# Kernel optimization log

Measured on AMD Instinct MI355X. Metric: run time of the kernel, lower is better.

The kernel has to match this reference:

```python
import jax, jax.numpy as jnp
import numpy as np

EMBED_DIM = 128
NUM_HEADS = 16
HEAD_DIM = EMBED_DIM // NUM_HEADS
SCALE = HEAD_DIM ** -0.5


def setup_inputs() -> dict:
    key = jax.random.key(0)
    ks = jax.random.split(key, 9)
    B, S, E = 4, 2048, EMBED_DIM
    s = 1.0 / np.sqrt(E)
    return {
        "x": jax.random.normal(ks[0], (B, S, E), dtype=jnp.float32),
        "Wq": jax.random.uniform(ks[1], (E, E), jnp.float32, -s, s),
        "bq": jax.random.uniform(ks[2], (E,), jnp.float32, -s, s),
        "Wk": jax.random.uniform(ks[3], (E, E), jnp.float32, -s, s),
        "bk": jax.random.uniform(ks[4], (E,), jnp.float32, -s, s),
        "Wv": jax.random.uniform(ks[5], (E, E), jnp.float32, -s, s),
        "bv": jax.random.uniform(ks[6], (E,), jnp.float32, -s, s),
        "Wo": jax.random.uniform(ks[7], (E, E), jnp.float32, -s, s),
        "bo": jax.random.uniform(ks[8], (E,), jnp.float32, -s, s),
    }


def reference(x, Wq, bq, Wk, bk, Wv, bv, Wo, bo):
    B, S, E = x.shape
    H, D = NUM_HEADS, HEAD_DIM
    # projections (torch Linear: x @ W.T + b)
    q = (x @ Wq.T + bq).reshape(B, S, H, D).transpose(0, 2, 1, 3)  # [B,H,S,D]
    k = (x @ Wk.T + bk).reshape(B, S, H, D).transpose(0, 2, 1, 3)
    v = (x @ Wv.T + bv).reshape(B, S, H, D).transpose(0, 2, 1, 3)
    scores = jnp.einsum("bhqd,bhkd->bhqk", q, k) * SCALE  # [B,H,S,S]
    causal_mask = jnp.triu(jnp.ones((S, S), dtype=bool), k=1)  # True above diag
    scores = jnp.where(causal_mask, jnp.float32(-1e9), scores)
    w = jax.nn.sigmoid(scores)
    w = w / jnp.sum(w, axis=-1, keepdims=True)  # sigmoid-sum normalization
    attn = jnp.einsum("bhqk,bhkd->bhqd", w, v)  # [B,H,S,D]
    attn = attn.transpose(0, 2, 1, 3).reshape(B, S, E)
    return attn @ Wo.T + bo
```

## Files before the change

### kernel.cpp

```cpp
#include <hip/hip_runtime.h>
#include <math.h>

#define EDIM 128
#define NHEAD 16
#define HDIM 8
#define SEQ 2048
#define BATCH 4
#define NROW (BATCH*SEQ)
#define QNEG (-0.35355339059327373f * 1.4426950408889634f)

#if __has_builtin(__builtin_amdgcn_exp2f)
#define EXP2F(x) __builtin_amdgcn_exp2f(x)
#else
#define EXP2F(x) exp2f(x)
#endif
#define RCPF(x) __builtin_amdgcn_rcpf(x)

typedef __attribute__((ext_vector_type(8))) short short8v;
typedef __attribute__((ext_vector_type(4))) short short4v;
typedef __attribute__((ext_vector_type(4))) float float4v;

union U16x8 { uint4 u; short8v s; };
union U16x4 { uint2 u; short4v s; };

#if __has_builtin(__builtin_amdgcn_mfma_f32_16x16x16bf16_1k)
#define MFMA_PV(a,b,c) __builtin_amdgcn_mfma_f32_16x16x16bf16_1k(a,b,c,0,0,0)
#else
static __device__ __forceinline__ float4v mfma_pv_asm(short4v a, short4v b, float4v c) {
  float4v d;
  asm("v_mfma_f32_16x16x16_bf16 %0, %1, %2, %3" : "=v"(d) : "v"(a), "v"(b), "v"(c));
  return d;
}
#define MFMA_PV(a,b,c) mfma_pv_asm(a,b,c)
#endif

__device__ __forceinline__ unsigned pk_bf16(float a, float b) {
  unsigned ua = __float_as_uint(a), ub = __float_as_uint(b);
  unsigned lo = (ua + 0x7fffu + ((ua >> 16) & 1u)) >> 16;
  unsigned hi = (ub + 0x7fffu + ((ub >> 16) & 1u)) & 0xffff0000u;
  return lo | hi;
}

__device__ __forceinline__
void afrags(const unsigned short* xs, int lq, int qd, short8v a[4])
{
  #pragma unroll
  for (int kk = 0; kk < 4; ++kk) {
    const unsigned addr =
        (unsigned)(lq * 256 + kk * 64 + qd * 16) ^ (unsigned)((lq & 7) << 4);
    a[kk] = *(const short8v*)((const char*)xs + addr);
  }
}

template<int MODE>
__device__ __forceinline__
void proj32(const float* __restrict__ X, const float* __restrict__ W,
            const float* __restrict__ bias, void* __restrict__ out,
            int row0, int tid,
            unsigned short* wlds, unsigned short* xs, unsigned short* bnc)
{
  {
    const int n = tid >> 1, h = (tid & 1) * 64;
    const float4* src = (const float4*)(W + (size_t)n * EDIM + h);
    const unsigned xr = (unsigned)((n & 7) << 4);
    #pragma unroll
    for (int j = 0; j < 8; ++j) {
      const float4 f0 = src[2 * j], f1 = src[2 * j + 1];
      const uint4 v = make_uint4(pk_bf16(f0.x, f0.y), pk_bf16(f0.z, f0.w),
                                 pk_bf16(f1.x, f1.y), pk_bf16(f1.z, f1.w));
      *(uint4*)((char*)wlds + ((unsigned)(n * 256 + h * 2 + j * 16) ^ xr)) = v;
    }
  }
  {
    const int r = tid >> 3, c = tid & 7;
    const float4* src = (const float4*)(X + (size_t)(row0 + r) * EDIM + c * 16);
    const unsigned xr = (unsigned)((r & 7) << 4);
    const float4 f0 = src[0], f1 = src[1], f2 = src[2], f3 = src[3];
    const uint4 v0 = make_uint4(pk_bf16(f0.x, f0.y), pk_bf16(f0.z, f0.w),
                                pk_bf16(f1.x, f1.y), pk_bf16(f1.z, f1.w));
    const uint4 v1 = make_uint4(pk_bf16(f2.x, f2.y), pk_bf16(f2.z, f2.w),
                                pk_bf16(f3.x, f3.y), pk_bf16(f3.z, f3.w));
    *(uint4*)((char*)xs + ((unsigned)(r * 256 + c * 32) ^ xr)) = v0;
    *(uint4*)((char*)xs + ((unsigned)(r * 256 + c * 32 + 16) ^ xr)) = v1;
  }
  __syncthreads();

  const int lane = tid & 63, wv = tid >> 6;
  const int lq = lane & 15, qd = lane >> 4;
  const int n0 = wv * 32;

  short8v b0[4], b1[4];
  #pragma unroll
  for (int kk = 0; kk < 4; ++kk) {
    const unsigned ad = (unsigned)((n0 + lq) * 256 + kk * 64 + qd * 16)
                      ^ (unsigned)((lq & 7) << 4);
    b0[kk] = *(const short8v*)((const char*)wlds + ad);
    b1[kk] = *(const short8v*)((const char*)wlds + ad + 4096);
  }

  const int nA = n0 + lq, nB = nA + 16;
  const float bzA = bias[nA], bzB = bias[nB];
  const int b_ = row0 >> 11;

  #pragma unroll
  for (int rt = 0; rt < 2; ++rt) {
    const int rowt = row0 + rt * 16;
    short8v a[4];
    afrags(xs + rt * 2048, lq, qd, a);

    float4v D0 = {0.f, 0.f, 0.f, 0.f}, D1 = {0.f, 0.f, 0.f, 0.f};
    #pragma unroll
    for (int kk = 0; kk < 4; ++kk) {
      D0 = __builtin_amdgcn_mfma_f32_16x16x32_bf16(a[kk], b0[kk], D0, 0, 0, 0);
      D1 = __builtin_amdgcn_mfma_f32_16x16x32_bf16(a[kk], b1[kk], D1, 0, 0, 0);
    }

    if (MODE == 3) {
      float* of = (float*)out + (size_t)(rowt + qd * 4) * EDIM + nA;
      #pragma unroll
      for (int r = 0; r < 4; ++r) {
        of[r * EDIM]      = D0[r] + bzA;
        of[r * EDIM + 16] = D1[r] + bzB;
      }
      continue;
    }

    const int srel = rowt & (SEQ - 1);

    if (MODE == 2) {
      const int tg = srel >> 4;
      unsigned short* oU = (unsigned short*)out;
      {
        const int bh = b_ * NHEAD + (nA >> 3), dv = nA & 7;
        uint2 p;
        p.x = pk_bf16(D0[0] + bzA, D0[1] + bzA);
        p.y = pk_bf16(D0[2] + bzA, D0[3] + bzA);
        *(uint2*)(oU + (size_t)bh * (SEQ * HDIM) + tg * 128 + dv * 16 + qd * 4) = p;
      }
      {
        const int bh = b_ * NHEAD + (nB >> 3), dv = nB & 7;
        uint2 p;
        p.x = pk_bf16(D1[0] + bzB, D1[1] + bzB);
        p.y = pk_bf16(D1[2] + bzB, D1[3] + bzB);
        *(uint2*)(oU + (size_t)bh * (SEQ * HDIM) + tg * 128 + dv * 16 + qd * 4) = p;
      }
      continue;
    }

    #pragma unroll
    for (int r = 0; r < 4; ++r) {
      float vA = D0[r] + bzA, vB = D1[r] + bzB;
      if (MODE == 0) { vA *= QNEG; vB *= QNEG; }
      const int m = qd * 4 + r;
      bnc[m * 20 + lq]       = (unsigned short)pk_bf16(vA, 0.f);
      bnc[320 + m * 20 + lq] = (unsigned short)pk_bf16(vB, 0.f);
    }
    __syncthreads();

    const int mm   = lane & 15;
    const int half = (lane >> 4) & 1;
    const int tile = lane >> 5;
    const unsigned short* sp = bnc + tile * 320 + mm * 20 + half * 8;
    const uint2 w0 = *(const uint2*)sp;
    const uint2 w1 = *(const uint2*)(sp + 4);
    const int bh = b_ * NHEAD + wv * 4 + tile * 2 + half;
    unsigned short* dp = (unsigned short*)out + ((size_t)bh * SEQ + srel + mm) * 8;
    *(uint4*)dp = make_uint4(w0.x, w0.y, w1.x, w1.y);
    __syncthreads();
  }
}

__global__ __launch_bounds__(256)
void qkv_kernel(const float* __restrict__ X,
                const float* __restrict__ Wq, const float* __restrict__ Wk,
                const float* __restrict__ Wv,
                const float* __restrict__ bq, const float* __restrict__ bk,
                const float* __restrict__ bv,
                unsigned* __restrict__ qb, unsigned* __restrict__ kb,
                unsigned* __restrict__ vb)
{
  __shared__ __align__(16) unsigned short wlds[16384];
  __shared__ __align__(16) unsigned short xs[4096];
  __shared__ __align__(16) unsigned short bnc[4 * 640];
  const int tid = threadIdx.x;
  const int row0 = blockIdx.x * 32;
  unsigned short* myb = bnc + (tid >> 6) * 640;
  const int m = blockIdx.y;
  if (m == 0)      proj32<0>(X, Wq, bq, (void*)qb, row0, tid, wlds, xs, myb);
  else if (m == 1) proj32<1>(X, Wk, bk, (void*)kb, row0, tid, wlds, xs, myb);
  else             proj32<2>(X, Wv, bv, (void*)vb, row0, tid, wlds, xs, myb);
}

__global__ __launch_bounds__(256)
void oproj_kernel(const float* __restrict__ A, const float* __restrict__ Wo,
                  const float* __restrict__ bo, float* __restrict__ out)
{
  __shared__ __align__(16) unsigned short wlds[16384];
  __shared__ __align__(16) unsigned short xs[4096];
  proj32<3>(A, Wo, bo, (void*)out, blockIdx.x * 32, threadIdx.x, wlds, xs, nullptr);
}

template<bool DIAG>
__device__ __forceinline__
float4v attn_step(short8v kf, short8v qf, short4v vf, float4v acc,
                  int laneq, int quad)
{
  const float4v z = {0.f, 0.f, 0.f, 0.f};
  float4v st = __builtin_amdgcn_mfma_f32_16x16x32_bf16(kf, qf, z, 0, 0, 0);
  unsigned rb[4];
  #pragma unroll
  for (int r = 0; r < 4; ++r) {
    float s = RCPF(1.f + EXP2F(st[r]));
    if (DIAG) s = (4 * quad + r <= laneq) ? s : 0.f;
    rb[r] = __float_as_uint(s) + 0x8000u;
  }
  U16x4 p;
  p.u.x = __builtin_amdgcn_perm(rb[1], rb[0], 0x07060302u);
  p.u.y = __builtin_amdgcn_perm(rb[3], rb[2], 0x07060302u);
  return MFMA_PV(p.s, vf, acc);
}

__device__ __forceinline__
short4v load_vfrag(const unsigned short* __restrict__ Vtbh, int t,
                   int quad, int d, bool is8)
{
  const unsigned short* p = Vtbh + t * 128 + d * 16 + 4 * quad;
  const uint2 v = *(const uint2*)p;
  U16x4 vf;
  vf.u.x = is8 ? 0x3F803F80u : v.x;
  vf.u.y = is8 ? 0x3F803F80u : v.y;
  return vf.s;
}

__device__ __forceinline__
void epilogue(float4v acc, int T, int bh, int laneq, int quad,
              float* __restrict__ out)
{
  const int b_ = bh >> 4, h = bh & 15;
  const int pidx = (quad * 16 + 8) << 2;
  #pragma unroll
  for (int r = 0; r < 4; ++r) {
    const float den = __int_as_float(
        __builtin_amdgcn_ds_bpermute(pidx, __float_as_int(acc[r])));
    const float val = acc[r] * RCPF(den);
    const int row = 16 * T + 4 * quad + r;
    if (laneq < 8)
      out[(size_t)(b_ * SEQ + row) * EDIM + h * HDIM + laneq] = val;
  }
}

__global__ __launch_bounds__(128, 8)
void attn_kernel(const unsigned* __restrict__ Qb, const unsigned* __restrict__ Kb,
                 const unsigned* __restrict__ Vb, float* __restrict__ out)
{
  __shared__ float cmb[2][64][4];

  const int bh    = blockIdx.x & 63;
  const int g     = blockIdx.x >> 6;
  const int w     = threadIdx.x >> 6;
  const int lane  = threadIdx.x & 63;
  const int laneq = lane & 15;
  const int quad  = lane >> 4;
  const int L = g, H = 127 - g;
  const int mL = (L + 1) >> 1, mH = (H + 1) >> 1;
  const int d   = laneq & 7;
  const bool is8 = (laneq == 8);

  const uint4* Kg = (const uint4*)Kb + (size_t)bh * 2048;
  const uint4* Qg = (const uint4*)Qb + (size_t)bh * 2048;
  const unsigned short* Vtbh = (const unsigned short*)Vb + (size_t)bh * SEQ * HDIM;

  U16x8 qfl, qfh;
  {
    const uint4 rl = Qg[16 * L + laneq];
    const uint4 rh = Qg[16 * H + laneq];
    qfl.u = (lane < 16) ? rl : make_uint4(0u, 0u, 0u, 0u);
    qfh.u = (lane < 16) ? rh : make_uint4(0u, 0u, 0u, 0u);
  }

  float4v accL = {0.f, 0.f, 0.f, 0.f};
  float4v accH = {0.f, 0.f, 0.f, 0.f};

  if (w == 0) {
    U16x8 kf; kf.u = Kg[laneq];
    short4v vf = load_vfrag(Vtbh, 0, quad, d, is8);
    #pragma unroll 2
    for (int t = 0; t < mH; ++t) {
      U16x8 kn; kn.u = Kg[16 * (t + 1) + laneq];
      short4v vn = load_vfrag(Vtbh, t + 1, quad, d, is8);
      if (t < mL) accL = attn_step<false>(kf.s, qfl.s, vf, accL, laneq, quad);
      accH = attn_step<false>(kf.s, qfh.s, vf, accH, laneq, quad);
      kf = kn; vf = vn;
    }
  } else {
    U16x8 kf; kf.u = Kg[16 * mL + laneq];
    short4v vf = load_vfrag(Vtbh, mL, quad, d, is8);
    #pragma unroll 2
    for (int t = mL; t < L; ++t) {
      U16x8 kn; kn.u = Kg[16 * (t + 1) + laneq];
      short4v vn = load_vfrag(Vtbh, t + 1, quad, d, is8);
      accL = attn_step<false>(kf.s, qfl.s, vf, accL, laneq, quad);
      kf = kn; vf = vn;
    }
    accL = attn_step<true>(kf.s, qfl.s, vf, accL, laneq, quad);
    kf.u = Kg[16 * mH + laneq];
    vf = load_vfrag(Vtbh, mH, quad, d, is8);
    #pragma unroll 2
    for (int t = mH; t < H; ++t) {
      U16x8 kn; kn.u = Kg[16 * (t + 1) + laneq];
      short4v vn = load_vfrag(Vtbh, t + 1, quad, d, is8);
      accH = attn_step<false>(kf.s, qfh.s, vf, accH, laneq, quad);
      kf = kn; vf = vn;
    }
    accH = attn_step<true>(kf.s, qfh.s, vf, accH, laneq, quad);

    *(float4*)&cmb[0][lane][0] = make_float4(accL[0], accL[1], accL[2], accL[3]);
    *(float4*)&cmb[1][lane][0] = make_float4(accH[0], accH[1], accH[2], accH[3]);
  }
  __syncthreads();

  if (w == 0) {
    const float4 pL = *(const float4*)&cmb[0][lane][0];
    const float4 pH = *(const float4*)&cmb[1][lane][0];
    accL[0] += pL.x; accL[1] += pL.y; accL[2] += pL.z; accL[3] += pL.w;
    accH[0] += pH.x; accH[1] += pH.y; accH[2] += pH.z; accH[3] += pH.w;
    epilogue(accL, L, bh, laneq, quad, out);
    epilogue(accH, H, bh, laneq, quad, out);
  }
}

extern "C" void kernel_launch(void* const* d_in, const int* in_sizes, int n_in,
                              void* d_out, int out_size, void* d_ws, size_t ws_size,
                              hipStream_t stream)
{
  const float* x  = (const float*)d_in[0];
  const float* Wq = (const float*)d_in[1];
  const float* bq = (const float*)d_in[2];
  const float* Wk = (const float*)d_in[3];
  const float* bk = (const float*)d_in[4];
  const float* Wv = (const float*)d_in[5];
  const float* bv = (const float*)d_in[6];
  const float* Wo = (const float*)d_in[7];
  const float* bo = (const float*)d_in[8];

  float* ws = (float*)d_ws;
  float*    attn = ws + 65536;
  unsigned* Qb   = (unsigned*)(ws + 65536 + 1048576);
  unsigned* Kb   = Qb + (size_t)524288;
  unsigned* Vb   = Kb + (size_t)524288;

  qkv_kernel<<<dim3(NROW / 32, 3), 256, 0, stream>>>(x, Wq, Wk, Wv, bq, bk, bv,
                                                     Qb, Kb, Vb);
  attn_kernel<<<dim3(4096), 128, 0, stream>>>(Qb, Kb, Vb, attn);
  oproj_kernel<<<dim3(NROW / 32), 256, 0, stream>>>(attn, Wo, bo, (float*)d_out);
}
```

Measured before the change: 121.8 us.

## Switch attention to 32x32x16 MFMA tiles with permlane32 swap for P

Rewrites the attention kernel to use 32x32 query/key tiles with the 32x32x16 bf16 MFMA for both scores and P·V, using permlane32_swap to rearrange the sigmoid probabilities into A-operand layout. Each block now handles a pair of 32-row tiles, and the combined key range is split evenly across two waves. This halves the grid, and the larger tiles are meant to raise MFMA efficiency per load. In exchange the kernel carries 16-register accumulators, lowers the occupancy hint to 4, and drops the explicit software prefetch of K/V.

```diff
diff --git a/kernel.cpp b/kernel.cpp
--- a/kernel.cpp
+++ b/kernel.cpp
@@ -19,26 +19,35 @@
 typedef __attribute__((ext_vector_type(8))) short short8v;
 typedef __attribute__((ext_vector_type(4))) short short4v;
 typedef __attribute__((ext_vector_type(4))) float float4v;
+typedef __attribute__((ext_vector_type(16))) float float16v;
 
 union U16x8 { uint4 u; short8v s; };
 union U16x4 { uint2 u; short4v s; };
 
-#if __has_builtin(__builtin_amdgcn_mfma_f32_16x16x16bf16_1k)
-#define MFMA_PV(a,b,c) __builtin_amdgcn_mfma_f32_16x16x16bf16_1k(a,b,c,0,0,0)
+#define MFMA32(a,b,c) __builtin_amdgcn_mfma_f32_32x32x16_bf16(a,b,c,0,0,0)
+
+__device__ __forceinline__ void lane32swap(unsigned &x, unsigned &y) {
+#if __has_builtin(__builtin_amdgcn_permlane32_swap)
+  typedef __attribute__((ext_vector_type(2))) unsigned uint2v;
+  uint2v r = __builtin_amdgcn_permlane32_swap(x, y, false, false);
+  x = r[0]; y = r[1];
 #else
-static __device__ __forceinline__ float4v mfma_pv_asm(short4v a, short4v b, float4v c) {
-  float4v d;
-  asm("v_mfma_f32_16x16x16_bf16 %0, %1, %2, %3" : "=v"(d) : "v"(a), "v"(b), "v"(c));
-  return d;
-}
-#define MFMA_PV(a,b,c) mfma_pv_asm(a,b,c)
+  asm volatile("v_permlane32_swap_b32 %0, %1" : "+v"(x), "+v"(y));
 #endif
+}
 
 __device__ __forceinline__ unsigned pk_bf16(float a, float b) {
   unsigned ua = __float_as_uint(a), ub = __float_as_uint(b);
   unsigned lo = (ua + 0x7fffu + ((ua >> 16) & 1u)) >> 16;
   unsigned hi = (ub + 0x7fffu + ((ub >> 16) & 1u)) & 0xffff0000u;
   return lo | hi;
+}
+
+__device__ __forceinline__ float16v zero16() {
+  float16v z;
+  #pragma unroll
+  for (int i = 0; i < 16; ++i) z[i] = 0.f;
+  return z;
 }
 
 __device__ __forceinline__
@@ -202,130 +211,145 @@
 
 template<bool DIAG>
 __device__ __forceinline__
-float4v attn_step(short8v kf, short8v qf, short4v vf, float4v acc,
-                  int laneq, int quad)
-{
-  const float4v z = {0.f, 0.f, 0.f, 0.f};
-  float4v st = __builtin_amdgcn_mfma_f32_16x16x32_bf16(kf, qf, z, 0, 0, 0);
-  unsigned rb[4];
-  #pragma unroll
-  for (int r = 0; r < 4; ++r) {
-    float s = RCPF(1.f + EXP2F(st[r]));
-    if (DIAG) s = (4 * quad + r <= laneq) ? s : 0.f;
-    rb[r] = __float_as_uint(s) + 0x8000u;
-  }
-  U16x4 p;
-  p.u.x = __builtin_amdgcn_perm(rb[1], rb[0], 0x07060302u);
-  p.u.y = __builtin_amdgcn_perm(rb[3], rb[2], 0x07060302u);
-  return MFMA_PV(p.s, vf, acc);
-}
-
-__device__ __forceinline__
-short4v load_vfrag(const unsigned short* __restrict__ Vtbh, int t,
-                   int quad, int d, bool is8)
-{
-  const unsigned short* p = Vtbh + t * 128 + d * 16 + 4 * quad;
-  const uint2 v = *(const uint2*)p;
-  U16x4 vf;
-  vf.u.x = is8 ? 0x3F803F80u : v.x;
-  vf.u.y = is8 ? 0x3F803F80u : v.y;
-  return vf.s;
-}
-
-__device__ __forceinline__
-void epilogue(float4v acc, int T, int bh, int laneq, int quad,
-              float* __restrict__ out)
+float16v step32(const uint4* __restrict__ Kg,
+                const unsigned short* __restrict__ Vtbh,
+                int t, U16x8 qf, float16v acc,
+                int lane, unsigned voff, bool is8)
+{
+  U16x8 kf; kf.u = Kg[32 * t + (lane & 31)];
+  const unsigned short* vt = Vtbh + 256 * t;
+  U16x8 v1, v2;
+  {
+    const uint4 a = *(const uint4*)(vt + voff);
+    const uint4 b = *(const uint4*)(vt + 128 + voff);
+    const uint4 ones = make_uint4(0x3F803F80u, 0x3F803F80u,
+                                  0x3F803F80u, 0x3F803F80u);
+    v1.u = is8 ? ones : a;
+    v2.u = is8 ? ones : b;
+  }
+
+  float16v st = MFMA32(kf.s, qf.s, zero16());
+
+  unsigned u[8];
+  #pragma unroll
+  for (int i = 0; i < 8; ++i) {
+    float s0 = RCPF(1.f + EXP2F(st[2 * i]));
+    float s1 = RCPF(1.f + EXP2F(st[2 * i + 1]));
+    if (DIAG) {
+      const int rb = ((2 * i) & 3) + 8 * (i >> 1) + ((lane >> 5) << 2);
+      const int q_ = lane & 31;
+      s0 = (rb     <= q_) ? s0 : 0.f;
+      s1 = (rb + 1 <= q_) ? s1 : 0.f;
+    }
+    const unsigned b0 = __float_as_uint(s0) + 0x8000u;
+    const unsigned b1 = __float_as_uint(s1) + 0x8000u;
+    u[i] = __builtin_amdgcn_perm(b1, b0, 0x07060302u);
+  }
+
+  lane32swap(u[0], u[2]);
+  lane32swap(u[1], u[3]);
+  lane32swap(u[4], u[6]);
+  lane32swap(u[5], u[7]);
+
+  U16x8 pa, pb;
+  pa.u = make_uint4(u[0], u[1], u[2], u[3]);
+  pb.u = make_uint4(u[4], u[5], u[6], u[7]);
+  acc = MFMA32(pa.s, v1.s, acc);
+  acc = MFMA32(pb.s, v2.s, acc);
+  return acc;
+}
+
+__device__ __forceinline__
+void seg32(const uint4* __restrict__ Kg, const unsigned short* __restrict__ Vtbh,
+           U16x8 qf, int T, int a, int b, float16v &acc,
+           int lane, unsigned voff, bool is8)
+{
+  if (a >= b) return;
+  const bool hasDiag = (b == T + 1);
+  const int e = hasDiag ? b - 1 : b;
+  for (int t = a; t < e; ++t)
+    acc = step32<false>(Kg, Vtbh, t, qf, acc, lane, voff, is8);
+  if (hasDiag)
+    acc = step32<true>(Kg, Vtbh, T, qf, acc, lane, voff, is8);
+}
+
+__device__ __forceinline__
+void epilogue32(float16v acc, int T, int bh, int lane, float* __restrict__ out)
 {
   const int b_ = bh >> 4, h = bh & 15;
-  const int pidx = (quad * 16 + 8) << 2;
-  #pragma unroll
-  for (int r = 0; r < 4; ++r) {
+  const int n = lane & 31;
+  const int pidx = ((lane & 32) | 8) << 2;
+  const int rowb = 32 * T + ((lane >> 5) << 2);
+  #pragma unroll
+  for (int reg = 0; reg < 16; ++reg) {
     const float den = __int_as_float(
-        __builtin_amdgcn_ds_bpermute(pidx, __float_as_int(acc[r])));
-    const float val = acc[r] * RCPF(den);
-    const int row = 16 * T + 4 * quad + r;
-    if (laneq < 8)
-      out[(size_t)(b_ * SEQ + row) * EDIM + h * HDIM + laneq] = val;
-  }
-}
-
-__global__ __launch_bounds__(128, 8)
+        __builtin_amdgcn_ds_bpermute(pidx, __float_as_int(acc[reg])));
+    const float val = acc[reg] * RCPF(den);
+    const int row = rowb + (reg & 3) + 8 * (reg >> 2);
+    if (n < 8)
+      out[(size_t)(b_ * SEQ + row) * EDIM + h * HDIM + n] = val;
+  }
+}
+
+__global__ __launch_bounds__(128, 4)
 void attn_kernel(const unsigned* __restrict__ Qb, const unsigned* __restrict__ Kb,
                  const unsigned* __restrict__ Vb, float* __restrict__ out)
 {
-  __shared__ float cmb[2][64][4];
-
-  const int bh    = blockIdx.x & 63;
-  const int g     = blockIdx.x >> 6;
-  const int w     = threadIdx.x >> 6;
-  const int lane  = threadIdx.x & 63;
-  const int laneq = lane & 15;
-  const int quad  = lane >> 4;
-  const int L = g, H = 127 - g;
-  const int mL = (L + 1) >> 1, mH = (H + 1) >> 1;
-  const int d   = laneq & 7;
-  const bool is8 = (laneq == 8);
+  __shared__ float cmb[2][64][16];
+
+  const int bh   = blockIdx.x & 63;
+  const int g    = blockIdx.x >> 6;
+  const int w    = threadIdx.x >> 6;
+  const int lane = threadIdx.x & 63;
+  const int L = g, H = 63 - g;
 
   const uint4* Kg = (const uint4*)Kb + (size_t)bh * 2048;
   const uint4* Qg = (const uint4*)Qb + (size_t)bh * 2048;
   const unsigned short* Vtbh = (const unsigned short*)Vb + (size_t)bh * SEQ * HDIM;
 
+  const unsigned voff = (unsigned)((lane & 7) * 16 + ((lane >> 5) << 3));
+  const bool is8 = (lane & 31) == 8;
+
   U16x8 qfl, qfh;
   {
-    const uint4 rl = Qg[16 * L + laneq];
-    const uint4 rh = Qg[16 * H + laneq];
-    qfl.u = (lane < 16) ? rl : make_uint4(0u, 0u, 0u, 0u);
-    qfh.u = (lane < 16) ? rh : make_uint4(0u, 0u, 0u, 0u);
-  }
-
-  float4v accL = {0.f, 0.f, 0.f, 0.f};
-  float4v accH = {0.f, 0.f, 0.f, 0.f};
+    const uint4 zz = make_uint4(0u, 0u, 0u, 0u);
+    qfl.u = (lane < 32) ? Qg[32 * L + lane] : zz;
+    qfh.u = (lane < 32) ? Qg[32 * H + lane] : zz;
+  }
+
+  float16v accL = zero16();
+  float16v accH = zero16();
+
+  const int st_ = w ? 32 : 0;
+  const int en_ = w ? 65 : 32;
+  const int Lp1 = L + 1;
+  const int aL = (st_ < Lp1) ? st_ : Lp1;
+  const int bL = (en_ < Lp1) ? en_ : Lp1;
+  int aH = st_ - Lp1; if (aH < 0) aH = 0;
+  int bH = en_ - Lp1; if (bH > H + 1) bH = H + 1;
+
+  seg32(Kg, Vtbh, qfl, L, aL, bL, accL, lane, voff, is8);
+  seg32(Kg, Vtbh, qfh, H, aH, bH, accH, lane, voff, is8);
+
+  if (w == 1) {
+    #pragma unroll
+    for (int i = 0; i < 4; ++i) {
+      *(float4*)&cmb[0][lane][4 * i] =
+          make_float4(accL[4*i], accL[4*i+1], accL[4*i+2], accL[4*i+3]);
+      *(float4*)&cmb[1][lane][4 * i] =
+          make_float4(accH[4*i], accH[4*i+1], accH[4*i+2], accH[4*i+3]);
+    }
+  }
+  __syncthreads();
 
   if (w == 0) {
-    U16x8 kf; kf.u = Kg[laneq];
-    short4v vf = load_vfrag(Vtbh, 0, quad, d, is8);
-    #pragma unroll 2
-    for (int t = 0; t < mH; ++t) {
-      U16x8 kn; kn.u = Kg[16 * (t + 1) + laneq];
-      short4v vn = load_vfrag(Vtbh, t + 1, quad, d, is8);
-      if (t < mL) accL = attn_step<false>(kf.s, qfl.s, vf, accL, laneq, quad);
-      accH = attn_step<false>(kf.s, qfh.s, vf, accH, laneq, quad);
-      kf = kn; vf = vn;
-    }
-  } else {
-    U16x8 kf; kf.u = Kg[16 * mL + laneq];
-    short4v vf = load_vfrag(Vtbh, mL, quad, d, is8);
-    #pragma unroll 2
-    for (int t = mL; t < L; ++t) {
-      U16x8 kn; kn.u = Kg[16 * (t + 1) + laneq];
-      short4v vn = load_vfrag(Vtbh, t + 1, quad, d, is8);
-      accL = attn_step<false>(kf.s, qfl.s, vf, accL, laneq, quad);
-      kf = kn; vf = vn;
-    }
-    accL = attn_step<true>(kf.s, qfl.s, vf, accL, laneq, quad);
-    kf.u = Kg[16 * mH + laneq];
-    vf = load_vfrag(Vtbh, mH, quad, d, is8);
-    #pragma unroll 2
-    for (int t = mH; t < H; ++t) {
-      U16x8 kn; kn.u = Kg[16 * (t + 1) + laneq];
-      short4v vn = load_vfrag(Vtbh, t + 1, quad, d, is8);
-      accH = attn_step<false>(kf.s, qfh.s, vf, accH, laneq, quad);
-      kf = kn; vf = vn;
-    }
-    accH = attn_step<true>(kf.s, qfh.s, vf, accH, laneq, quad);
-
-    *(float4*)&cmb[0][lane][0] = make_float4(accL[0], accL[1], accL[2], accL[3]);
-    *(float4*)&cmb[1][lane][0] = make_float4(accH[0], accH[1], accH[2], accH[3]);
-  }
-  __syncthreads();
-
-  if (w == 0) {
-    const float4 pL = *(const float4*)&cmb[0][lane][0];
-    const float4 pH = *(const float4*)&cmb[1][lane][0];
-    accL[0] += pL.x; accL[1] += pL.y; accL[2] += pL.z; accL[3] += pL.w;
-    accH[0] += pH.x; accH[1] += pH.y; accH[2] += pH.z; accH[3] += pH.w;
-    epilogue(accL, L, bh, laneq, quad, out);
-    epilogue(accH, H, bh, laneq, quad, out);
+    #pragma unroll
+    for (int i = 0; i < 16; ++i) {
+      accL[i] += cmb[0][lane][i];
+      accH[i] += cmb[1][lane][i];
+    }
+    epilogue32(accL, L, bh, lane, out);
+    epilogue32(accH, H, bh, lane, out);
   }
 }
 
@@ -351,6 +375,6 @@
 
   qkv_kernel<<<dim3(NROW / 32, 3), 256, 0, stream>>>(x, Wq, Wk, Wv, bq, bk, bv,
                                                      Qb, Kb, Vb);
-  attn_kernel<<<dim3(4096), 128, 0, stream>>>(Qb, Kb, Vb, attn);
+  attn_kernel<<<dim3(2048), 128, 0, stream>>>(Qb, Kb, Vb, attn);
   oproj_kernel<<<dim3(NROW / 32), 256, 0, stream>>>(attn, Wo, bo, (float*)d_out);
 }
```

Measured after the change: 124.4 us. 2.1% more time.
